# Kernel optimization log

Hardware: AMD Instinct MI355X
Metric: run time of the kernel (lower is better)

## Reference

```python
import jax, jax.numpy as jnp
import numpy as np

N = 100000
K = 32
F_IN = 64
DIMS = [64, 64, 64]

def setup_inputs() -> dict:
    key = jax.random.key(0)
    ks = jax.random.split(key, 10)
    x = jax.random.normal(ks[0], (N, F_IN), dtype=jnp.float32)
    neighbour_indices = jax.random.randint(ks[1], (N, K), 0, N, dtype=jnp.int32)
    distancesq = jax.random.uniform(ks[2], (N, K), dtype=jnp.float32)
    # Dense params: layer 0 takes F_IN; layers i>0 take 2*DIMS[i-1]
    in_dims = [F_IN] + [2 * d for d in DIMS[:-1]]
    params = {}
    for i, (din, dout) in enumerate(zip(in_dims, DIMS)):
        params[f"W{i}"] = jax.random.normal(ks[3 + i], (din, dout), dtype=jnp.float32) * (1.0 / np.sqrt(din))
        params[f"b{i}"] = jnp.zeros((dout,), dtype=jnp.float32)
    return {"x": x, "neighbour_indices": neighbour_indices, "distancesq": distancesq, **params}

def _accumulate_knn(distances, features, indices):
    # distances: [N,K] (already scaled by 10), features: [N,F], indices: [N,K]
    w = jnp.exp(-distances)[..., None]              # [N,K,1]
    g = features[indices]                           # [N,K,F] gather
    wg = w * g
    fmean = jnp.mean(wg, axis=1)                    # [N,F]
    fmax = jnp.max(wg, axis=1)                      # [N,F]
    return jnp.concatenate([fmean, fmax], axis=1)   # [N,2F]

def reference(x, neighbour_indices, distancesq, W0, b0, W1, b1, W2, b2):
    Ws = [W0, W1, W2]
    bs = [b0, b1, b2]
    feats = x
    allfeat = []
    for W, b in zip(Ws, bs):
        feats = jax.nn.relu(feats @ W + b)          # [N,D]
        prev = feats
        feats = _accumulate_knn(10.0 * distancesq, feats, neighbour_indices)  # [N,2D]
        feats = feats - jnp.tile(prev, (1, 2))
        allfeat.append(feats)
    return jnp.concatenate(allfeat + [x], axis=-1)  # [N, F_IN + 2*sum(DIMS)]
```

## Files before the change

kernel.cpp:

```cpp
#include <hip/hip_runtime.h>
#include <math.h>

#define N_NODES    100000
#define K_NEIGH    32
#define OUT_STRIDE 448

static __device__ __forceinline__ unsigned short f2bf(float f) {
    unsigned int u = __float_as_uint(f);
    unsigned int r = (u + 0x7FFFu + ((u >> 16) & 1u)) >> 16;
    return (unsigned short)r;
}
static __device__ __forceinline__ float bf2f(unsigned short h) {
    return __uint_as_float(((unsigned int)h) << 16);
}

template <int DIN, bool COPY_X>
__global__ __launch_bounds__(256) void dense_kernel(
    const float* __restrict__ in, int in_stride,
    const float* __restrict__ W, const float* __restrict__ b,
    unsigned short* __restrict__ F, float* __restrict__ out)
{
    __shared__ float aT[DIN][65];

    const int tid  = threadIdx.x;
    const int row0 = blockIdx.x * 64;

    for (int i = tid; i < 64 * DIN; i += 256) {
        const int r = i >> (DIN == 64 ? 6 : 7);
        const int c = i & (DIN - 1);
        const int n = row0 + r;
        float v = 0.f;
        if (n < N_NODES) {
            v = in[(size_t)n * in_stride + c];
            if (COPY_X) out[(size_t)n * OUT_STRIDE + 384 + c] = v;
        }
        aT[c][r] = v;
    }
    __syncthreads();

    const int lane = tid & 63;
    const int c0   = __builtin_amdgcn_readfirstlane((tid >> 6) * 16);
    const int n    = row0 + lane;

    float acc[16];
#pragma unroll
    for (int c = 0; c < 16; ++c) acc[c] = b[c0 + c];

#pragma unroll 4
    for (int k = 0; k < DIN; ++k) {
        const float a = aT[k][lane];
        const float* __restrict__ wrow = &W[(size_t)k * 64 + c0];
#pragma unroll
        for (int c = 0; c < 16; ++c)
            acc[c] = fmaf(a, wrow[c], acc[c]);
    }

    if (n < N_NODES) {
        unsigned int u[8];
#pragma unroll
        for (int c = 0; c < 16; c += 2) {
            const unsigned int lo = f2bf(fmaxf(acc[c], 0.f));
            const unsigned int hi = f2bf(fmaxf(acc[c + 1], 0.f));
            u[c >> 1] = lo | (hi << 16);
        }
        uint4* dst = (uint4*)&F[(size_t)n * 64 + c0];
        dst[0] = make_uint4(u[0], u[1], u[2], u[3]);
        dst[1] = make_uint4(u[4], u[5], u[6], u[7]);
    }
}

__global__ __launch_bounds__(256) void acc_kernel(
    const unsigned short* __restrict__ F,
    const int* __restrict__ idx,
    const float* __restrict__ dist,
    float* __restrict__ out)
{
    const int wave = threadIdx.x >> 6;
    const int lane = threadIdx.x & 63;
    const int n = blockIdx.x * 4 + wave;
    if (n >= N_NODES) return;

    int   jv = 0;
    float wv = 0.f;
    if (lane < 32) {
        jv = idx[(size_t)n * K_NEIGH + lane];
        wv = __expf(-10.f * dist[(size_t)n * K_NEIGH + lane]);
    }

    const float prev = bf2f(F[(size_t)n * 64 + lane]);
    float sum = 0.f;
    float mx  = -INFINITY;

#pragma unroll 8
    for (int k = 0; k < K_NEIGH; ++k) {
        const int   jk = __shfl(jv, k);
        const float wk = __shfl(wv, k);
        const float g  = bf2f(F[(size_t)jk * 64 + lane]);
        const float v  = wk * g;
        sum += v;
        mx = fmaxf(mx, v);
    }

    out[(size_t)n * OUT_STRIDE + lane]      = sum * (1.f / 32.f) - prev;
    out[(size_t)n * OUT_STRIDE + 64 + lane] = mx - prev;
}

extern "C" void kernel_launch(void* const* d_in, const int* in_sizes, int n_in,
                              void* d_out, int out_size, void* d_ws, size_t ws_size,
                              hipStream_t stream)
{
    const float* x    = (const float*)d_in[0];
    const int*   idx  = (const int*)  d_in[1];
    const float* dist = (const float*)d_in[2];
    const float* W0   = (const float*)d_in[3];
    const float* b0   = (const float*)d_in[4];
    const float* W1   = (const float*)d_in[5];
    const float* b1   = (const float*)d_in[6];
    const float* W2   = (const float*)d_in[7];
    const float* b2   = (const float*)d_in[8];

    float* out = (float*)d_out;
    unsigned short* F = (unsigned short*)d_ws;

    const int dense_grid = (N_NODES + 63) / 64;
    const int acc_grid   = N_NODES / 4;

    dense_kernel<64, true><<<dense_grid, 256, 0, stream>>>(x, 64, W0, b0, F, out);
    acc_kernel<<<acc_grid, 256, 0, stream>>>(F, idx, dist, out + 0);

    dense_kernel<128, false><<<dense_grid, 256, 0, stream>>>(out + 0, OUT_STRIDE, W1, b1, F, nullptr);
    acc_kernel<<<acc_grid, 256, 0, stream>>>(F, idx, dist, out + 128);

    dense_kernel<128, false><<<dense_grid, 256, 0, stream>>>(out + 128, OUT_STRIDE, W2, b2, F, nullptr);
    acc_kernel<<<acc_grid, 256, 0, stream>>>(F, idx, dist, out + 256);
}
```

Measured before the change: 505.6 us.

## Use bf16 MFMA for dense layers and precompute exp distance weights once

The dense layers move from per-lane scalar FMA loops to 16x16x32 bf16 MFMA instructions. Inputs and transposed weights are staged in LDS as bf16, and a new prep kernel converts the weights. The same prep kernel computes exp(-10*dist) once into a workspace table, so the three accumulation passes read it instead of recomputing it. The accumulation kernel now loads the index and weight scalars directly (uniform loads) instead of using lane shuffles. In exchange, the dense inputs are rounded to bf16, the output stores become scattered 2-byte writes, and there is an extra launch plus extra table traffic.

```diff
diff --git a/kernel.cpp b/kernel.cpp
--- a/kernel.cpp
+++ b/kernel.cpp
@@ -5,96 +5,120 @@
 #define K_NEIGH    32
 #define OUT_STRIDE 448
 
+typedef __attribute__((ext_vector_type(8))) __bf16 bf16x8;
+typedef __attribute__((ext_vector_type(4))) float  f32x4;
+
 static __device__ __forceinline__ unsigned short f2bf(float f) {
     unsigned int u = __float_as_uint(f);
-    unsigned int r = (u + 0x7FFFu + ((u >> 16) & 1u)) >> 16;
-    return (unsigned short)r;
+    return (unsigned short)((u + 0x7FFFu + ((u >> 16) & 1u)) >> 16);
 }
 static __device__ __forceinline__ float bf2f(unsigned short h) {
     return __uint_as_float(((unsigned int)h) << 16);
 }
 
+__global__ __launch_bounds__(256) void prep_kernel(
+    const float* __restrict__ dist, float* __restrict__ wtab,
+    const float* __restrict__ W0, const float* __restrict__ W1,
+    const float* __restrict__ W2,
+    unsigned short* __restrict__ Wt0, unsigned short* __restrict__ Wt1,
+    unsigned short* __restrict__ Wt2)
+{
+    const int i = blockIdx.x * 256 + threadIdx.x;
+    if (i < N_NODES * K_NEIGH) wtab[i] = __expf(-10.f * dist[i]);
+    if (i < 64 * 64)  Wt0[(i & 63) * 64  + (i >> 6)] = f2bf(W0[i]);
+    if (i < 128 * 64) Wt1[(i & 63) * 128 + (i >> 6)] = f2bf(W1[i]);
+    if (i < 128 * 64) Wt2[(i & 63) * 128 + (i >> 6)] = f2bf(W2[i]);
+}
+
 template <int DIN, bool COPY_X>
 __global__ __launch_bounds__(256) void dense_kernel(
     const float* __restrict__ in, int in_stride,
-    const float* __restrict__ W, const float* __restrict__ b,
+    const unsigned short* __restrict__ Wt,
+    const float* __restrict__ b,
     unsigned short* __restrict__ F, float* __restrict__ out)
 {
-    __shared__ float aT[DIN][65];
+    constexpr int LDK = DIN + 8;
+    __shared__ unsigned short aLDS[64 * LDK];
+    __shared__ unsigned short bLDS[64 * LDK];
 
     const int tid  = threadIdx.x;
     const int row0 = blockIdx.x * 64;
 
-    for (int i = tid; i < 64 * DIN; i += 256) {
-        const int r = i >> (DIN == 64 ? 6 : 7);
-        const int c = i & (DIN - 1);
+    for (int i = tid; i < 64 * (DIN / 4); i += 256) {
+        const int r = i / (DIN / 4);
+        const int c = (i % (DIN / 4)) * 4;
         const int n = row0 + r;
-        float v = 0.f;
+        float4 v = make_float4(0.f, 0.f, 0.f, 0.f);
         if (n < N_NODES) {
-            v = in[(size_t)n * in_stride + c];
-            if (COPY_X) out[(size_t)n * OUT_STRIDE + 384 + c] = v;
+            v = *(const float4*)&in[(size_t)n * in_stride + c];
+            if (COPY_X) *(float4*)&out[(size_t)n * OUT_STRIDE + 384 + c] = v;
         }
-        aT[c][r] = v;
+        const unsigned int u0 = (unsigned int)f2bf(v.x) | ((unsigned int)f2bf(v.y) << 16);
+        const unsigned int u1 = (unsigned int)f2bf(v.z) | ((unsigned int)f2bf(v.w) << 16);
+        *(uint2*)&aLDS[r * LDK + c] = make_uint2(u0, u1);
+    }
+    for (int i = tid; i < 64 * (DIN / 8); i += 256) {
+        const int nn = i / (DIN / 8);
+        const int k0 = (i % (DIN / 8)) * 8;
+        *(uint4*)&bLDS[nn * LDK + k0] = *(const uint4*)&Wt[nn * DIN + k0];
     }
     __syncthreads();
 
     const int lane = tid & 63;
-    const int c0   = __builtin_amdgcn_readfirstlane((tid >> 6) * 16);
-    const int n    = row0 + lane;
+    const int wv   = tid >> 6;
+    const int m    = lane & 15;
+    const int quad = lane >> 4;
 
-    float acc[16];
+    f32x4 acc[4];
 #pragma unroll
-    for (int c = 0; c < 16; ++c) acc[c] = b[c0 + c];
+    for (int nb = 0; nb < 4; ++nb) acc[nb] = (f32x4){0.f, 0.f, 0.f, 0.f};
 
-#pragma unroll 4
-    for (int k = 0; k < DIN; ++k) {
-        const float a = aT[k][lane];
-        const float* __restrict__ wrow = &W[(size_t)k * 64 + c0];
 #pragma unroll
-        for (int c = 0; c < 16; ++c)
-            acc[c] = fmaf(a, wrow[c], acc[c]);
+    for (int ks = 0; ks < DIN / 32; ++ks) {
+        const int koff = ks * 32 + quad * 8;
+        const bf16x8 afr =
+            *reinterpret_cast<const bf16x8*>(&aLDS[(wv * 16 + m) * LDK + koff]);
+#pragma unroll
+        for (int nb = 0; nb < 4; ++nb) {
+            const bf16x8 bfr =
+                *reinterpret_cast<const bf16x8*>(&bLDS[(nb * 16 + m) * LDK + koff]);
+            acc[nb] = __builtin_amdgcn_mfma_f32_16x16x32_bf16(afr, bfr, acc[nb], 0, 0, 0);
+        }
     }
 
-    if (n < N_NODES) {
-        unsigned int u[8];
 #pragma unroll
-        for (int c = 0; c < 16; c += 2) {
-            const unsigned int lo = f2bf(fmaxf(acc[c], 0.f));
-            const unsigned int hi = f2bf(fmaxf(acc[c + 1], 0.f));
-            u[c >> 1] = lo | (hi << 16);
+    for (int nb = 0; nb < 4; ++nb) {
+        const int c    = nb * 16 + m;
+        const float bc = b[c];
+#pragma unroll
+        for (int reg = 0; reg < 4; ++reg) {
+            const int n = row0 + wv * 16 + quad * 4 + reg;
+            if (n < N_NODES) {
+                const float vv = fmaxf(acc[nb][reg] + bc, 0.f);
+                F[(size_t)n * 64 + c] = f2bf(vv);
+            }
         }
-        uint4* dst = (uint4*)&F[(size_t)n * 64 + c0];
-        dst[0] = make_uint4(u[0], u[1], u[2], u[3]);
-        dst[1] = make_uint4(u[4], u[5], u[6], u[7]);
     }
 }
 
 __global__ __launch_bounds__(256) void acc_kernel(
     const unsigned short* __restrict__ F,
     const int* __restrict__ idx,
-    const float* __restrict__ dist,
+    const float* __restrict__ wtab,
     float* __restrict__ out)
 {
-    const int wave = threadIdx.x >> 6;
+    const int wv   = __builtin_amdgcn_readfirstlane(threadIdx.x >> 6);
     const int lane = threadIdx.x & 63;
-    const int n = blockIdx.x * 4 + wave;
-    if (n >= N_NODES) return;
-
-    int   jv = 0;
-    float wv = 0.f;
-    if (lane < 32) {
-        jv = idx[(size_t)n * K_NEIGH + lane];
-        wv = __expf(-10.f * dist[(size_t)n * K_NEIGH + lane]);
-    }
+    const int n    = blockIdx.x * 4 + wv;
 
     const float prev = bf2f(F[(size_t)n * 64 + lane]);
     float sum = 0.f;
     float mx  = -INFINITY;
 
-#pragma unroll 8
+#pragma unroll
     for (int k = 0; k < K_NEIGH; ++k) {
-        const int   jk = __shfl(jv, k);
-        const float wk = __shfl(wv, k);
+        const int   jk = idx [(size_t)n * K_NEIGH + k];
+        const float wk = wtab[(size_t)n * K_NEIGH + k];
         const float g  = bf2f(F[(size_t)jk * 64 + lane]);
         const float v  = wk * g;
         sum += v;
@@ -120,17 +144,26 @@
     const float* b2   = (const float*)d_in[8];
 
     float* out = (float*)d_out;
-    unsigned short* F = (unsigned short*)d_ws;
 
+    char* ws = (char*)d_ws;
+    unsigned short* F    = (unsigned short*)(ws);
+    float*          wtab = (float*)         (ws + 12800000);
+    unsigned short* Wt0  = (unsigned short*)(ws + 25600000);
+    unsigned short* Wt1  = (unsigned short*)(ws + 25608192);
+    unsigned short* Wt2  = (unsigned short*)(ws + 25624576);
+
+    const int prep_grid  = (N_NODES * K_NEIGH + 255) / 256;
     const int dense_grid = (N_NODES + 63) / 64;
     const int acc_grid   = N_NODES / 4;
 
-    dense_kernel<64, true><<<dense_grid, 256, 0, stream>>>(x, 64, W0, b0, F, out);
-    acc_kernel<<<acc_grid, 256, 0, stream>>>(F, idx, dist, out + 0);
+    prep_kernel<<<prep_grid, 256, 0, stream>>>(dist, wtab, W0, W1, W2, Wt0, Wt1, Wt2);
 
-    dense_kernel<128, false><<<dense_grid, 256, 0, stream>>>(out + 0, OUT_STRIDE, W1, b1, F, nullptr);
-    acc_kernel<<<acc_grid, 256, 0, stream>>>(F, idx, dist, out + 128);
+    dense_kernel<64, true><<<dense_grid, 256, 0, stream>>>(x, 64, Wt0, b0, F, out);
+    acc_kernel<<<acc_grid, 256, 0, stream>>>(F, idx, wtab, out + 0);
 
-    dense_kernel<128, false><<<dense_grid, 256, 0, stream>>>(out + 128, OUT_STRIDE, W2, b2, F, nullptr);
-    acc_kernel<<<acc_grid, 256, 0, stream>>>(F, idx, dist, out + 256);
+    dense_kernel<128, false><<<dense_grid, 256, 0, stream>>>(out + 0, OUT_STRIDE, Wt1, b1, F, nullptr);
+    acc_kernel<<<acc_grid, 256, 0, stream>>>(F, idx, wtab, out + 128);
+
+    dense_kernel<128, false><<<dense_grid, 256, 0, stream>>>(out + 128, OUT_STRIDE, Wt2, b2, F, nullptr);
+    acc_kernel<<<acc_grid, 256, 0, stream>>>(F, idx, wtab, out + 256);
 }
```

Result: faster. 422.3 us (-16.5%).
